# Optimization experiments

Hardware: AMD Instinct MI355X
Metric: run time of the kernel (lower is better)

## Reference

```python
import jax, jax.numpy as jnp
import numpy as np
import math

N = 50000
E = 600000
HID = 128
NG = 50
NF = 128
CUTOFF = 10.0
OFFSET = 0.0


def ssp(x):
    # shifted softplus, standard SchNet activation
    return jax.nn.softplus(x) - jnp.log(2.0).astype(x.dtype)


def setup_inputs() -> dict:
    key = jax.random.key(0)
    ks = jax.random.split(key, 12)
    x = jax.random.normal(ks[0], (N, HID), dtype=jnp.float32)
    ji_pairs = jax.random.randint(ks[1], (2, E), 0, N, dtype=jnp.int64)
    e_ji = jax.random.uniform(ks[2], (E,), dtype=jnp.float32) * CUTOFF
    e_ji_basis = jax.random.normal(ks[3], (E, NG), dtype=jnp.float32)
    # filter_nn: Linear(NG, NF) -> ssp -> Linear(NF, NF)
    fw1 = jax.random.normal(ks[4], (NF, NG), dtype=jnp.float32) * (1.0 / np.sqrt(NG))
    fb1 = jnp.zeros((NF,), jnp.float32)
    fw2 = jax.random.normal(ks[5], (NF, NF), dtype=jnp.float32) * (1.0 / np.sqrt(NF))
    fb2 = jnp.zeros((NF,), jnp.float32)
    # CFConv linear1 (no bias), linear2
    w1 = jax.random.normal(ks[6], (NF, HID), dtype=jnp.float32) * (1.0 / np.sqrt(HID))
    w2 = jax.random.normal(ks[7], (HID, NF), dtype=jnp.float32) * (1.0 / np.sqrt(NF))
    b2 = jnp.zeros((HID,), jnp.float32)
    # InteractionBlock linear3
    w3 = jax.random.normal(ks[8], (HID, HID), dtype=jnp.float32) * (1.0 / np.sqrt(HID))
    b3 = jnp.zeros((HID,), jnp.float32)
    return {"x": x, "ji_pairs": ji_pairs, "e_ji": e_ji, "e_ji_basis": e_ji_basis,
            "fw1": fw1, "fb1": fb1, "fw2": fw2, "fb2": fb2,
            "w1": w1, "w2": w2, "b2": b2, "w3": w3, "b3": b3}


def reference(x, ji_pairs, e_ji, e_ji_basis, fw1, fb1, fw2, fb2, w1, w2, b2, w3, b3):
    # cosine cutoff  [E]
    C = 0.25 * (jnp.cos((e_ji - OFFSET) * (np.pi / (CUTOFF - OFFSET))) + 1.0)
    # filter MLP on edge basis  [E, NF]
    h = ssp(e_ji_basis @ fw1.T + fb1)
    W = (h @ fw2.T + fb2) * C[:, None]
    # node projection  [N, NF]
    xh = x @ w1.T
    # gather x_j, modulate by W, scatter-add to target nodes (PyG source_to_target)
    src, dst = ji_pairs[0], ji_pairs[1]
    msg = xh[src] * W                                # [E, NF]
    agg = jax.ops.segment_sum(msg, dst, num_segments=N)  # [N, NF]
    out = agg @ w2.T + b2                            # [N, HID]
    out = ssp(out)
    out = out @ w3.T + b3
    return out
```

## Files before the change

### kernel.cpp

```cpp
#include <hip/hip_runtime.h>

typedef float f32x4 __attribute__((ext_vector_type(4)));
typedef short bf16x8 __attribute__((ext_vector_type(8)));
typedef unsigned short u16;
typedef unsigned int u32;

__device__ __forceinline__ u32 cvt_pk_bf16(float lo, float hi) {
    u32 r;
    asm("v_cvt_pk_bf16_f32 %0, %1, %2" : "=v"(r) : "v"(lo), "v"(hi));
    return r;
}

__device__ __forceinline__ u16 f2b(float f) {
    union { float f; u32 u; } v; v.f = f;
    u32 r = v.u + 0x7fffu + ((v.u >> 16) & 1u);
    return (u16)(r >> 16);
}
__device__ __forceinline__ float b2f_lo(u32 p) {
    union { u32 u; float f; } v; v.u = p << 16; return v.f;
}
__device__ __forceinline__ float b2f_hi(u32 p) {
    union { u32 u; float f; } v; v.u = p & 0xffff0000u; return v.f;
}

__device__ __forceinline__ float ssp(float x) {
    return fmaxf(x, 0.0f) + __logf(1.0f + __expf(-fabsf(x))) - 0.6931471805599453f;
}

__global__ void prep_weights(const float* __restrict__ fw1,
                             const float* __restrict__ fw2,
                             const float* __restrict__ w1,
                             const float* __restrict__ w2,
                             const float* __restrict__ w3,
                             u16* __restrict__ out) {
    int t = blockIdx.x * blockDim.x + threadIdx.x;
    if (t < 128 * 64) {
        int c = t >> 6, k = t & 63;
        out[t] = f2b(k < 50 ? fw1[c * 50 + k] : 0.0f);
        return;
    }
    t -= 128 * 64;
    if (t < 16384) { out[8192 + t] = f2b(fw2[t]); return; }
    t -= 16384;
    if (t < 16384) { out[8192 + 16384 + t] = f2b(w1[t]); return; }
    t -= 16384;
    if (t < 16384) { out[8192 + 32768 + t] = f2b(w2[t]); return; }
    t -= 16384;
    if (t < 16384) { out[8192 + 49152 + t] = f2b(w3[t]); return; }
}

template <int ACT, int OBF>
__global__ __launch_bounds__(256, 3) void linear128(
    const float* __restrict__ in, const u16* __restrict__ wb,
    const float* __restrict__ bias, void* __restrict__ outv, int M) {
    __shared__ u16 in_lds[64 * 136];
    __shared__ u16 w_lds[128 * 136];

    const int tid = threadIdx.x;
    const int r0 = blockIdx.x * 64;

    for (int idx = tid; idx < 128 * 16; idx += 256) {
        int c = idx >> 4, kc = (idx & 15) * 8;
        *reinterpret_cast<uint4*>(&w_lds[c * 136 + kc]) =
            *reinterpret_cast<const uint4*>(&wb[c * 128 + kc]);
    }
    for (int idx = tid; idx < 64 * 32; idx += 256) {
        int r = idx >> 5, kc = (idx & 31) * 4;
        int row = r0 + r;
        float4 v = make_float4(0.f, 0.f, 0.f, 0.f);
        if (row < M) v = *reinterpret_cast<const float4*>(&in[(size_t)row * 128 + kc]);
        u32* p = reinterpret_cast<u32*>(&in_lds[r * 136 + kc]);
        p[0] = cvt_pk_bf16(v.x, v.y); p[1] = cvt_pk_bf16(v.z, v.w);
    }
    __syncthreads();

    const int l = tid & 63, w = tid >> 6;
    const int lr = l & 15, lg = l >> 4;

    f32x4 acc[8] = {};
    for (int ks = 0; ks < 4; ++ks) {
        bf16x8 a = *reinterpret_cast<const bf16x8*>(
            &in_lds[(w * 16 + lr) * 136 + ks * 32 + lg * 8]);
        for (int n = 0; n < 8; ++n) {
            bf16x8 b = *reinterpret_cast<const bf16x8*>(
                &w_lds[(n * 16 + lr) * 136 + ks * 32 + lg * 8]);
            acc[n] = __builtin_amdgcn_mfma_f32_16x16x32_bf16(a, b, acc[n], 0, 0, 0);
        }
    }

    for (int n = 0; n < 8; ++n) {
        int c = n * 16 + lr;
        float bv = bias ? bias[c] : 0.0f;
        for (int i = 0; i < 4; ++i) {
            int row = r0 + w * 16 + lg * 4 + i;
            if (row < M) {
                float v = acc[n][i] + bv;
                if (ACT) v = ssp(v);
                if (OBF) ((u16*)outv)[(size_t)row * 128 + c] = f2b(v);
                else     ((float*)outv)[(size_t)row * 128 + c] = v;
            }
        }
    }
}

__global__ __launch_bounds__(512) void edge_mlp(
    const float* __restrict__ basis, const float* __restrict__ e_ji,
    const u16* __restrict__ fw1b, const u16* __restrict__ fw2b,
    const float* __restrict__ fb1, const float* __restrict__ fb2,
    const int* __restrict__ epos, u16* __restrict__ Wb,
    int E, int nTiles, int stride) {
    __shared__ u16 bas[2][32 * 72];
    __shared__ u16 hb[2][32 * 136];

    const int tid = threadIdx.x;
    const int l = tid & 63, w = tid >> 6;
    const int lr = l & 15, lg = l >> 4;
    const int c8 = lg * 8, c4 = lg * 4;

    bf16x8 wa1[2], wa2[4];
    const u16* p1 = &fw1b[(size_t)(w * 16 + lr) * 64];
    wa1[0] = *reinterpret_cast<const bf16x8*>(p1 + c8);
    wa1[1] = *reinterpret_cast<const bf16x8*>(p1 + 32 + c8);
    const u16* p2 = &fw2b[(size_t)(w * 16 + lr) * 128];
#pragma unroll
    for (int ks = 0; ks < 4; ++ks)
        wa2[ks] = *reinterpret_cast<const bf16x8*>(p2 + ks * 32 + c8);
    const float4 b1v = *reinterpret_cast<const float4*>(&fb1[w * 16 + c4]);
    const float4 b2v = *reinterpret_cast<const float4*>(&fb2[w * 16 + c4]);

    for (int idx = tid; idx < 2 * 32 * 7; idx += 512) {
        int b = idx / 224, rem = idx - b * 224;
        int row = rem / 7, q = rem - row * 7;
        *reinterpret_cast<u32*>(&bas[b][row * 72 + 50 + 2 * q]) = 0u;
    }

    const int srow = tid & 31, cb = tid >> 5;
    const bool has2 = cb < 9;

    int it = blockIdx.x;
    if (it >= nTiles) return;

    {
        int er = it * 32 + srow; if (er >= E) er = E - 1;
        const float* rp = &basis[(size_t)er * 50];
        float2 v0 = *reinterpret_cast<const float2*>(rp + 2 * cb);
        *reinterpret_cast<u32*>(&bas[0][srow * 72 + 2 * cb]) = cvt_pk_bf16(v0.x, v0.y);
        if (has2) {
            float2 v1 = *reinterpret_cast<const float2*>(rp + 2 * (cb + 16));
            *reinterpret_cast<u32*>(&bas[0][srow * 72 + 2 * (cb + 16)]) =
                cvt_pk_bf16(v1.x, v1.y);
        }
    }
    __syncthreads();

    int buf = 0;
    for (; it < nTiles; it += stride, buf ^= 1) {
        const int nxt = it + stride;
        const bool hn = nxt < nTiles;
        float2 stg0, stg1;
        if (hn) {
            int er = nxt * 32 + srow; if (er >= E) er = E - 1;
            const float* rp = &basis[(size_t)er * 50];
            stg0 = *reinterpret_cast<const float2*>(rp + 2 * cb);
            if (has2) stg1 = *reinterpret_cast<const float2*>(rp + 2 * (cb + 16));
        }
        const int er0 = it * 32 + lr, er1 = er0 + 16;
        const int ec0 = er0 < E ? er0 : E - 1;
        const int ec1 = er1 < E ? er1 : E - 1;
        const int ep0 = epos[ec0], ep1 = epos[ec1];
        const float ej0 = e_ji[ec0], ej1 = e_ji[ec1];

        f32x4 acc1[2] = {};
#pragma unroll
        for (int ks = 0; ks < 2; ++ks) {
            bf16x8 bb0 = *reinterpret_cast<const bf16x8*>(
                &bas[buf][lr * 72 + ks * 32 + c8]);
            bf16x8 bb1 = *reinterpret_cast<const bf16x8*>(
                &bas[buf][(16 + lr) * 72 + ks * 32 + c8]);
            acc1[0] = __builtin_amdgcn_mfma_f32_16x16x32_bf16(wa1[ks], bb0, acc1[0], 0, 0, 0);
            acc1[1] = __builtin_amdgcn_mfma_f32_16x16x32_bf16(wa1[ks], bb1, acc1[1], 0, 0, 0);
        }
#pragma unroll
        for (int t = 0; t < 2; ++t) {
            u32* d = reinterpret_cast<u32*>(
                &hb[buf][(t * 16 + lr) * 136 + w * 16 + c4]);
            d[0] = cvt_pk_bf16(ssp(acc1[t][0] + b1v.x), ssp(acc1[t][1] + b1v.y));
            d[1] = cvt_pk_bf16(ssp(acc1[t][2] + b1v.z), ssp(acc1[t][3] + b1v.w));
        }
        if (hn) {
            *reinterpret_cast<u32*>(&bas[buf ^ 1][srow * 72 + 2 * cb]) =
                cvt_pk_bf16(stg0.x, stg0.y);
            if (has2)
                *reinterpret_cast<u32*>(&bas[buf ^ 1][srow * 72 + 2 * (cb + 16)]) =
                    cvt_pk_bf16(stg1.x, stg1.y);
        }
        __syncthreads();

        f32x4 acc2[2] = {};
#pragma unroll
        for (int ks = 0; ks < 4; ++ks) {
            bf16x8 hb0 = *reinterpret_cast<const bf16x8*>(
                &hb[buf][lr * 136 + ks * 32 + c8]);
            bf16x8 hb1 = *reinterpret_cast<const bf16x8*>(
                &hb[buf][(16 + lr) * 136 + ks * 32 + c8]);
            acc2[0] = __builtin_amdgcn_mfma_f32_16x16x32_bf16(wa2[ks], hb0, acc2[0], 0, 0, 0);
            acc2[1] = __builtin_amdgcn_mfma_f32_16x16x32_bf16(wa2[ks], hb1, acc2[1], 0, 0, 0);
        }
#pragma unroll
        for (int t = 0; t < 2; ++t) {
            const int er = t == 0 ? er0 : er1;
            if (er < E) {
                const float ej = t == 0 ? ej0 : ej1;
                const int pos = t == 0 ? ep0 : ep1;
                const float cv = 0.25f * (__cosf(ej * 0.31415926535897932f) + 1.0f);
                uint2 pk;
                pk.x = cvt_pk_bf16((acc2[t][0] + b2v.x) * cv,
                                   (acc2[t][1] + b2v.y) * cv);
                pk.y = cvt_pk_bf16((acc2[t][2] + b2v.z) * cv,
                                   (acc2[t][3] + b2v.w) * cv);
                *reinterpret_cast<uint2*>(
                    &Wb[(size_t)pos * 128 + w * 16 + c4]) = pk;
            }
        }
    }
}

__global__ __launch_bounds__(256) void fused_tail(
    const u16* __restrict__ aggb, const u16* __restrict__ w2b,
    const u16* __restrict__ w3b, const float* __restrict__ b2,
    const float* __restrict__ b3, float* __restrict__ out,
    int N, int nTiles, int stride) {
    __shared__ u16 bas[2][32 * 136];
    __shared__ u16 hb[2][32 * 136];

    const int tid = threadIdx.x;
    const int l = tid & 63, w = tid >> 6;
    const int lr = l & 15, lg = l >> 4;
    const int c8 = lg * 8, c4 = lg * 4;

    bf16x8 wA[2][4], wB[2][4];
    float4 b2v[2], b3v[2];
#pragma unroll
    for (int i = 0; i < 2; ++i) {
        const u16* pA = &w2b[(size_t)((w * 2 + i) * 16 + lr) * 128];
        const u16* pB = &w3b[(size_t)((w * 2 + i) * 16 + lr) * 128];
#pragma unroll
        for (int ks = 0; ks < 4; ++ks) {
            wA[i][ks] = *reinterpret_cast<const bf16x8*>(pA + ks * 32 + c8);
            wB[i][ks] = *reinterpret_cast<const bf16x8*>(pB + ks * 32 + c8);
        }
        b2v[i] = *reinterpret_cast<const float4*>(&b2[(w * 2 + i) * 16 + c4]);
        b3v[i] = *reinterpret_cast<const float4*>(&b3[(w * 2 + i) * 16 + c4]);
    }

    const int srow = tid & 31, cb = tid >> 5;

    int it = blockIdx.x;
    if (it >= nTiles) return;

    {
        int nd = it * 32 + srow; if (nd >= N) nd = N - 1;
        *reinterpret_cast<uint4*>(&bas[0][srow * 136 + cb * 8]) =
            *reinterpret_cast<const uint4*>(&aggb[(size_t)nd * 128 + cb * 8]);
        *reinterpret_cast<uint4*>(&bas[0][srow * 136 + 64 + cb * 8]) =
            *reinterpret_cast<const uint4*>(&aggb[(size_t)nd * 128 + 64 + cb * 8]);
    }
    __syncthreads();

    int buf = 0;
    for (; it < nTiles; it += stride, buf ^= 1) {
        const int nxt = it + stride;
        const bool hn = nxt < nTiles;
        uint4 stg0, stg1;
        if (hn) {
            int nd = nxt * 32 + srow; if (nd >= N) nd = N - 1;
            stg0 = *reinterpret_cast<const uint4*>(&aggb[(size_t)nd * 128 + cb * 8]);
            stg1 = *reinterpret_cast<const uint4*>(&aggb[(size_t)nd * 128 + 64 + cb * 8]);
        }

        f32x4 acc1[2][2] = {};
#pragma unroll
        for (int ks = 0; ks < 4; ++ks) {
            bf16x8 bb0 = *reinterpret_cast<const bf16x8*>(
                &bas[buf][lr * 136 + ks * 32 + c8]);
            bf16x8 bb1 = *reinterpret_cast<const bf16x8*>(
                &bas[buf][(16 + lr) * 136 + ks * 32 + c8]);
#pragma unroll
            for (int i = 0; i < 2; ++i) {
                acc1[0][i] = __builtin_amdgcn_mfma_f32_16x16x32_bf16(wA[i][ks], bb0, acc1[0][i], 0, 0, 0);
                acc1[1][i] = __builtin_amdgcn_mfma_f32_16x16x32_bf16(wA[i][ks], bb1, acc1[1][i], 0, 0, 0);
            }
        }
#pragma unroll
        for (int t = 0; t < 2; ++t) {
#pragma unroll
            for (int i = 0; i < 2; ++i) {
                u32* d = reinterpret_cast<u32*>(
                    &hb[buf][(t * 16 + lr) * 136 + (w * 2 + i) * 16 + c4]);
                d[0] = cvt_pk_bf16(ssp(acc1[t][i][0] + b2v[i].x),
                                   ssp(acc1[t][i][1] + b2v[i].y));
                d[1] = cvt_pk_bf16(ssp(acc1[t][i][2] + b2v[i].z),
                                   ssp(acc1[t][i][3] + b2v[i].w));
            }
        }
        if (hn) {
            *reinterpret_cast<uint4*>(&bas[buf ^ 1][srow * 136 + cb * 8]) = stg0;
            *reinterpret_cast<uint4*>(&bas[buf ^ 1][srow * 136 + 64 + cb * 8]) = stg1;
        }
        __syncthreads();

        f32x4 acc2[2][2] = {};
#pragma unroll
        for (int ks = 0; ks < 4; ++ks) {
            bf16x8 hb0 = *reinterpret_cast<const bf16x8*>(
                &hb[buf][lr * 136 + ks * 32 + c8]);
            bf16x8 hb1 = *reinterpret_cast<const bf16x8*>(
                &hb[buf][(16 + lr) * 136 + ks * 32 + c8]);
#pragma unroll
            for (int i = 0; i < 2; ++i) {
                acc2[0][i] = __builtin_amdgcn_mfma_f32_16x16x32_bf16(wB[i][ks], hb0, acc2[0][i], 0, 0, 0);
                acc2[1][i] = __builtin_amdgcn_mfma_f32_16x16x32_bf16(wB[i][ks], hb1, acc2[1][i], 0, 0, 0);
            }
        }
#pragma unroll
        for (int t = 0; t < 2; ++t) {
            int nd = it * 32 + t * 16 + lr;
            if (nd < N) {
#pragma unroll
                for (int i = 0; i < 2; ++i) {
                    float4 o;
                    o.x = acc2[t][i][0] + b3v[i].x;
                    o.y = acc2[t][i][1] + b3v[i].y;
                    o.z = acc2[t][i][2] + b3v[i].z;
                    o.w = acc2[t][i][3] + b3v[i].w;
                    *reinterpret_cast<float4*>(
                        &out[(size_t)nd * 128 + (w * 2 + i) * 16 + c4]) = o;
                }
            }
        }
    }
}

__global__ void hist_kernel(const int* __restrict__ pairs, int* __restrict__ deg, int E) {
    int e = blockIdx.x * blockDim.x + threadIdx.x;
    if (e < E) atomicAdd(&deg[pairs[E + e]], 1);
}

__global__ void scan_a(const int* __restrict__ deg, int* __restrict__ incl,
                       int* __restrict__ bsum, int N) {
    __shared__ int s[256];
    int i = blockIdx.x * 256 + threadIdx.x;
    int v = (i < N) ? deg[i] : 0;
    s[threadIdx.x] = v; __syncthreads();
    for (int off = 1; off < 256; off <<= 1) {
        int t = (threadIdx.x >= off) ? s[threadIdx.x - off] : 0;
        __syncthreads();
        s[threadIdx.x] += t; __syncthreads();
    }
    if (i < N) incl[i] = s[threadIdx.x];
    if (threadIdx.x == 255) bsum[blockIdx.x] = s[255];
}

__global__ void scan_b(int* __restrict__ bsum, int nb) {
    __shared__ int s[256];
    int v = (threadIdx.x < nb) ? bsum[threadIdx.x] : 0;
    s[threadIdx.x] = v; __syncthreads();
    for (int off = 1; off < 256; off <<= 1) {
        int t = (threadIdx.x >= off) ? s[threadIdx.x - off] : 0;
        __syncthreads();
        s[threadIdx.x] += t; __syncthreads();
    }
    if (threadIdx.x < nb) bsum[threadIdx.x] = s[threadIdx.x] - v;
}

__global__ void scan_c(const int* __restrict__ incl, const int* __restrict__ deg,
                       const int* __restrict__ bsum, int* __restrict__ rowst,
                       int* __restrict__ cursor, int N) {
    int i = blockIdx.x * 256 + threadIdx.x;
    if (i < N) {
        int r = incl[i] - deg[i] + bsum[blockIdx.x];
        rowst[i] = r; cursor[i] = r;
    }
}

__global__ void fill_kernel(const int* __restrict__ pairs, int* __restrict__ cursor,
                            int* __restrict__ esrc, int* __restrict__ epos, int E) {
    int e = blockIdx.x * blockDim.x + threadIdx.x;
    if (e < E) {
        int s = pairs[e], d = pairs[E + e];
        int pos = atomicAdd(&cursor[d], 1);
        esrc[pos] = s;
        epos[e] = pos;
    }
}

__global__ __launch_bounds__(256) void aggregate(
    const u16* __restrict__ Wb, const u16* __restrict__ xhb,
    const int* __restrict__ rowst, const int* __restrict__ deg,
    const int* __restrict__ esrc, u16* __restrict__ aggb, int N) {
    const int w = threadIdx.x >> 6, lane = threadIdx.x & 63;
    const int n = blockIdx.x * 4 + w;
    if (n >= N) return;
    const int rs = rowst[n], d = deg[n];
    const int g = lane >> 4;
    const int co = (lane & 15) * 8;
    float acc[8] = {0.f, 0.f, 0.f, 0.f, 0.f, 0.f, 0.f, 0.f};
    const int nq = (d + 3) >> 2;
    const int dm1 = d > 0 ? d - 1 : 0;

    int srcn = (d > 0) ? esrc[rs + (g < d ? g : dm1)] : 0;
    for (int q = 0; q < nq; ++q) {
        const int k = q * 4 + g;
        const bool val = k < d;
        const int row = rs + (val ? k : dm1);
        const int src = srcn;
        const int kn = (q + 1) * 4 + g;
        if (q + 1 < nq) srcn = esrc[rs + (kn < d ? kn : dm1)];

        uint4 wp = *reinterpret_cast<const uint4*>(&Wb[(size_t)row * 128 + co]);
        uint4 xp = *reinterpret_cast<const uint4*>(&xhb[(size_t)src * 128 + co]);
        if (val) {
            const u32* wu = reinterpret_cast<const u32*>(&wp);
            const u32* xu = reinterpret_cast<const u32*>(&xp);
#pragma unroll
            for (int c = 0; c < 4; ++c) {
                acc[2 * c]     = fmaf(b2f_lo(xu[c]), b2f_lo(wu[c]), acc[2 * c]);
                acc[2 * c + 1] = fmaf(b2f_hi(xu[c]), b2f_hi(wu[c]), acc[2 * c + 1]);
            }
        }
    }
#pragma unroll
    for (int c = 0; c < 8; ++c) {
        float v = acc[c];
        v += __shfl_xor(v, 16);
        v += __shfl_xor(v, 32);
        acc[c] = v;
    }
    if (g == 0) {
        uint4 pk;
        pk.x = cvt_pk_bf16(acc[0], acc[1]);
        pk.y = cvt_pk_bf16(acc[2], acc[3]);
        pk.z = cvt_pk_bf16(acc[4], acc[5]);
        pk.w = cvt_pk_bf16(acc[6], acc[7]);
        *reinterpret_cast<uint4*>(&aggb[(size_t)n * 128 + co]) = pk;
    }
}

__global__ __launch_bounds__(256, 2) void edge_kernel(
    const float* __restrict__ basis, const float* __restrict__ e_ji,
    const int* __restrict__ pairs, const float* __restrict__ xh,
    const u16* __restrict__ fw1b, const u16* __restrict__ fw2b,
    const float* __restrict__ fb1, const float* __restrict__ fb2,
    float* __restrict__ agg, int E) {
    __shared__ u16 hb[64 * 136];
    __shared__ u16 fw1_lds[128 * 72];
    __shared__ u16 fw2_lds[128 * 136];
    __shared__ float cc[64];
    __shared__ int s_src[64];
    __shared__ int s_dst[64];

    const int tid = threadIdx.x;
    const int e0 = blockIdx.x * 64;

    for (int idx = tid; idx < 128 * 8; idx += 256) {
        int c = idx >> 3, kc = (idx & 7) * 8;
        *reinterpret_cast<uint4*>(&fw1_lds[c * 72 + kc]) =
            *reinterpret_cast<const uint4*>(&fw1b[c * 64 + kc]);
    }
    for (int idx = tid; idx < 128 * 16; idx += 256) {
        int c = idx >> 4, kc = (idx & 15) * 8;
        *reinterpret_cast<uint4*>(&fw2_lds[c * 136 + kc]) =
            *reinterpret_cast<const uint4*>(&fw2b[c * 128 + kc]);
    }
    for (int idx = tid; idx < 64 * 64; idx += 256) {
        int e = idx >> 6, k = idx & 63;
        int eg = e0 + e;
        float v = (k < 50 && eg < E) ? basis[(size_t)eg * 50 + k] : 0.0f;
        hb[e * 72 + k] = f2b(v);
    }
    if (tid < 64) {
        int eg = e0 + tid;
        if (eg < E) {
            cc[tid] = 0.25f * (__cosf(e_ji[eg] * 0.31415926535897932f) + 1.0f);
            s_src[tid] = pairs[eg];
            s_dst[tid] = pairs[E + eg];
        } else { cc[tid] = 0.0f; s_src[tid] = 0; s_dst[tid] = 0; }
    }
    __syncthreads();

    const int l = tid & 63, w = tid >> 6;
    const int lr = l & 15, lg = l >> 4;

    f32x4 acc1[8] = {};
    for (int ks = 0; ks < 2; ++ks) {
        bf16x8 a = *reinterpret_cast<const bf16x8*>(
            &hb[(w * 16 + lr) * 72 + ks * 32 + lg * 8]);
        for (int n = 0; n < 8; ++n) {
            bf16x8 b = *reinterpret_cast<const bf16x8*>(
                &fw1_lds[(n * 16 + lr) * 72 + ks * 32 + lg * 8]);
            acc1[n] = __builtin_amdgcn_mfma_f32_16x16x32_bf16(a, b, acc1[n], 0, 0, 0);
        }
    }
    __syncthreads();

    for (int n = 0; n < 8; ++n) {
        int c = n * 16 + lr;
        float bv = fb1[c];
        for (int i = 0; i < 4; ++i) {
            int r = w * 16 + lg * 4 + i;
            hb[r * 136 + c] = f2b(ssp(acc1[n][i] + bv));
        }
    }
    __syncthreads();

    f32x4 acc2[8] = {};
    for (int ks = 0; ks < 4; ++ks) {
        bf16x8 a = *reinterpret_cast<const bf16x8*>(
            &hb[(w * 16 + lr) * 136 + ks * 32 + lg * 8]);
        for (int n = 0; n < 8; ++n) {
            bf16x8 b = *reinterpret_cast<const bf16x8*>(
                &fw2_lds[(n * 16 + lr) * 136 + ks * 32 + lg * 8]);
            acc2[n] = __builtin_amdgcn_mfma_f32_16x16x32_bf16(a, b, acc2[n], 0, 0, 0);
        }
    }

    for (int n = 0; n < 8; ++n) {
        int c = n * 16 + lr;
        float bv = fb2[c];
        for (int i = 0; i < 4; ++i) {
            int eloc = w * 16 + lg * 4 + i;
            if (e0 + eloc < E) {
                float Wv = (acc2[n][i] + bv) * cc[eloc];
                float val = xh[(size_t)s_src[eloc] * 128 + c] * Wv;
                unsafeAtomicAdd(&agg[(size_t)s_dst[eloc] * 128 + c], val);
            }
        }
    }
}

extern "C" void kernel_launch(void* const* d_in, const int* in_sizes, int n_in,
                              void* d_out, int out_size, void* d_ws, size_t ws_size,
                              hipStream_t stream) {
    const float* x      = (const float*)d_in[0];
    const int*   pairs  = (const int*)d_in[1];
    const float* e_ji   = (const float*)d_in[2];
    const float* basis  = (const float*)d_in[3];
    const float* fw1    = (const float*)d_in[4];
    const float* fb1    = (const float*)d_in[5];
    const float* fw2    = (const float*)d_in[6];
    const float* fb2    = (const float*)d_in[7];
    const float* w1     = (const float*)d_in[8];
    const float* w2     = (const float*)d_in[9];
    const float* b2     = (const float*)d_in[10];
    const float* w3     = (const float*)d_in[11];
    const float* b3     = (const float*)d_in[12];
    float* out = (float*)d_out;

    const int N = in_sizes[0] / 128;
    const int E = in_sizes[2];
    const int nodeBlocks = (N + 63) / 64;
    const int nchunks = (N + 255) / 256;
    char* ws = (char*)d_ws;

    size_t off = 0;
    auto nxt = [&](size_t bytes) {
        size_t o = off; off = (off + bytes + 255) & ~(size_t)255; return o;
    };
    u16*   Wb     = (u16*)  (ws + nxt((size_t)E * 128 * 2));
    u16*   xhb    = (u16*)  (ws + nxt((size_t)N * 128 * 2));
    u16*   aggb   = (u16*)  (ws + nxt((size_t)N * 128 * 2));
    u16*   wb     = (u16*)  (ws + nxt(81920 * 2));
    int*   deg    = (int*)  (ws + nxt((size_t)N * 4));
    int*   incl   = (int*)  (ws + nxt((size_t)N * 4));
    int*   rowst  = (int*)  (ws + nxt((size_t)N * 4));
    int*   cursor = (int*)  (ws + nxt((size_t)N * 4));
    int*   bsum   = (int*)  (ws + nxt(1024));
    int*   esrc   = (int*)  (ws + nxt((size_t)E * 4));
    int*   epos   = (int*)  (ws + nxt((size_t)E * 4));
    const size_t needed = off;

    const u16* fw1b = wb;
    const u16* fw2b = wb + 8192;
    const u16* w1b  = wb + 8192 + 16384;
    const u16* w2b  = wb + 8192 + 32768;
    const u16* w3b  = wb + 8192 + 49152;

    if (ws_size >= needed && nchunks <= 256) {
        prep_weights<<<288, 256, 0, stream>>>(fw1, fw2, w1, w2, w3, wb);
        hipMemsetAsync(deg, 0, (size_t)N * 4, stream);

        linear128<0, 1><<<nodeBlocks, 256, 0, stream>>>(x, w1b, nullptr, xhb, N);

        hist_kernel<<<(E + 255) / 256, 256, 0, stream>>>(pairs, deg, E);
        scan_a<<<nchunks, 256, 0, stream>>>(deg, incl, bsum, N);
        scan_b<<<1, 256, 0, stream>>>(bsum, nchunks);
        scan_c<<<nchunks, 256, 0, stream>>>(incl, deg, bsum, rowst, cursor, N);
        fill_kernel<<<(E + 255) / 256, 256, 0, stream>>>(pairs, cursor, esrc, epos, E);

        const int nTiles = (E + 31) / 32;
        const int gridE = nTiles < 1024 ? nTiles : 1024;
        edge_mlp<<<gridE, 512, 0, stream>>>(basis, e_ji, fw1b, fw2b,
                                            fb1, fb2, epos, Wb, E, nTiles, gridE);

        aggregate<<<(N + 3) / 4, 256, 0, stream>>>(Wb, xhb, rowst, deg,
                                                   esrc, aggb, N);

        const int ntT = (N + 31) / 32;
        const int gridT = ntT < 1024 ? ntT : 1024;
        fused_tail<<<gridT, 256, 0, stream>>>(aggb, w2b, w3b, b2, b3, out,
                                              N, ntT, gridT);
    } else {
        const size_t nodeBytes = (size_t)N * 128 * sizeof(float);
        float* xhf   = (float*)ws;
        float* aggf  = (float*)(ws + nodeBytes);
        u16*   wbf   = (u16*)(ws + 2 * nodeBytes);
        const u16* ffw1b = wbf;
        const u16* ffw2b = wbf + 8192;
        const u16* fw1bw = wbf + 8192 + 16384;
        const u16* fw2bw = wbf + 8192 + 32768;
        const u16* fw3bw = wbf + 8192 + 49152;

        prep_weights<<<288, 256, 0, stream>>>(fw1, fw2, w1, w2, w3, wbf);
        hipMemsetAsync(aggf, 0, nodeBytes, stream);
        linear128<0, 0><<<nodeBlocks, 256, 0, stream>>>(x, fw1bw, nullptr, xhf, N);
        edge_kernel<<<(E + 63) / 64, 256, 0, stream>>>(basis, e_ji, pairs, xhf,
                                                       ffw1b, ffw2b, fb1, fb2, aggf, E);
        linear128<1, 0><<<nodeBlocks, 256, 0, stream>>>(aggf, fw2bw, b2, out, N);
        linear128<0, 0><<<nodeBlocks, 256, 0, stream>>>(out, fw3bw, b3, out, N);
    }
}
```

Baseline: 264.6 us.

## Fuse source-node gather and message multiply into edge MLP epilogue

The edge MLP now gathers the projected source-node features itself and writes the full message (xh[src] * W) in CSR order. The aggregate kernel then only sums message rows, so it no longer needs the esrc index array or a second random gather, and the fill kernel stops writing esrc. The cost is that edge_mlp does random gathers of xh (small uint2 reads per lane) in its hot loop, and the product is rounded to bf16 once before summation.

```diff
diff --git a/kernel.cpp b/kernel.cpp
--- a/kernel.cpp
+++ b/kernel.cpp
@@ -105,9 +105,10 @@
 
 __global__ __launch_bounds__(512) void edge_mlp(
     const float* __restrict__ basis, const float* __restrict__ e_ji,
+    const int* __restrict__ pairs, const u16* __restrict__ xhb,
     const u16* __restrict__ fw1b, const u16* __restrict__ fw2b,
     const float* __restrict__ fb1, const float* __restrict__ fb2,
-    const int* __restrict__ epos, u16* __restrict__ Wb,
+    const int* __restrict__ epos, u16* __restrict__ Mb,
     int E, int nTiles, int stride) {
     __shared__ u16 bas[2][32 * 72];
     __shared__ u16 hb[2][32 * 136];
@@ -169,6 +170,11 @@
         const int ec1 = er1 < E ? er1 : E - 1;
         const int ep0 = epos[ec0], ep1 = epos[ec1];
         const float ej0 = e_ji[ec0], ej1 = e_ji[ec1];
+        const int src0 = pairs[ec0], src1 = pairs[ec1];
+        const uint2 xv0 = *reinterpret_cast<const uint2*>(
+            &xhb[(size_t)src0 * 128 + w * 16 + c4]);
+        const uint2 xv1 = *reinterpret_cast<const uint2*>(
+            &xhb[(size_t)src1 * 128 + w * 16 + c4]);
 
         f32x4 acc1[2] = {};
 #pragma unroll
@@ -212,14 +218,17 @@
             if (er < E) {
                 const float ej = t == 0 ? ej0 : ej1;
                 const int pos = t == 0 ? ep0 : ep1;
+                const uint2 xv = t == 0 ? xv0 : xv1;
                 const float cv = 0.25f * (__cosf(ej * 0.31415926535897932f) + 1.0f);
+                float m0 = b2f_lo(xv.x) * ((acc2[t][0] + b2v.x) * cv);
+                float m1 = b2f_hi(xv.x) * ((acc2[t][1] + b2v.y) * cv);
+                float m2 = b2f_lo(xv.y) * ((acc2[t][2] + b2v.z) * cv);
+                float m3 = b2f_hi(xv.y) * ((acc2[t][3] + b2v.w) * cv);
                 uint2 pk;
-                pk.x = cvt_pk_bf16((acc2[t][0] + b2v.x) * cv,
-                                   (acc2[t][1] + b2v.y) * cv);
-                pk.y = cvt_pk_bf16((acc2[t][2] + b2v.z) * cv,
-                                   (acc2[t][3] + b2v.w) * cv);
+                pk.x = cvt_pk_bf16(m0, m1);
+                pk.y = cvt_pk_bf16(m2, m3);
                 *reinterpret_cast<uint2*>(
-                    &Wb[(size_t)pos * 128 + w * 16 + c4]) = pk;
+                    &Mb[(size_t)pos * 128 + w * 16 + c4]) = pk;
             }
         }
     }
@@ -384,20 +393,18 @@
 }
 
 __global__ void fill_kernel(const int* __restrict__ pairs, int* __restrict__ cursor,
-                            int* __restrict__ esrc, int* __restrict__ epos, int E) {
+                            int* __restrict__ epos, int E) {
     int e = blockIdx.x * blockDim.x + threadIdx.x;
     if (e < E) {
-        int s = pairs[e], d = pairs[E + e];
+        int d = pairs[E + e];
         int pos = atomicAdd(&cursor[d], 1);
-        esrc[pos] = s;
         epos[e] = pos;
     }
 }
 
 __global__ __launch_bounds__(256) void aggregate(
-    const u16* __restrict__ Wb, const u16* __restrict__ xhb,
-    const int* __restrict__ rowst, const int* __restrict__ deg,
-    const int* __restrict__ esrc, u16* __restrict__ aggb, int N) {
+    const u16* __restrict__ Mb, const int* __restrict__ rowst,
+    const int* __restrict__ deg, u16* __restrict__ aggb, int N) {
     const int w = threadIdx.x >> 6, lane = threadIdx.x & 63;
     const int n = blockIdx.x * 4 + w;
     if (n >= N) return;
@@ -408,24 +415,17 @@
     const int nq = (d + 3) >> 2;
     const int dm1 = d > 0 ? d - 1 : 0;
 
-    int srcn = (d > 0) ? esrc[rs + (g < d ? g : dm1)] : 0;
     for (int q = 0; q < nq; ++q) {
         const int k = q * 4 + g;
         const bool val = k < d;
         const int row = rs + (val ? k : dm1);
-        const int src = srcn;
-        const int kn = (q + 1) * 4 + g;
-        if (q + 1 < nq) srcn = esrc[rs + (kn < d ? kn : dm1)];
-
-        uint4 wp = *reinterpret_cast<const uint4*>(&Wb[(size_t)row * 128 + co]);
-        uint4 xp = *reinterpret_cast<const uint4*>(&xhb[(size_t)src * 128 + co]);
+        uint4 mp = *reinterpret_cast<const uint4*>(&Mb[(size_t)row * 128 + co]);
         if (val) {
-            const u32* wu = reinterpret_cast<const u32*>(&wp);
-            const u32* xu = reinterpret_cast<const u32*>(&xp);
+            const u32* mu = reinterpret_cast<const u32*>(&mp);
 #pragma unroll
             for (int c = 0; c < 4; ++c) {
-                acc[2 * c]     = fmaf(b2f_lo(xu[c]), b2f_lo(wu[c]), acc[2 * c]);
-                acc[2 * c + 1] = fmaf(b2f_hi(xu[c]), b2f_hi(wu[c]), acc[2 * c + 1]);
+                acc[2 * c]     += b2f_lo(mu[c]);
+                acc[2 * c + 1] += b2f_hi(mu[c]);
             }
         }
     }
@@ -566,7 +566,7 @@
     auto nxt = [&](size_t bytes) {
         size_t o = off; off = (off + bytes + 255) & ~(size_t)255; return o;
     };
-    u16*   Wb     = (u16*)  (ws + nxt((size_t)E * 128 * 2));
+    u16*   Mb     = (u16*)  (ws + nxt((size_t)E * 128 * 2));
     u16*   xhb    = (u16*)  (ws + nxt((size_t)N * 128 * 2));
     u16*   aggb   = (u16*)  (ws + nxt((size_t)N * 128 * 2));
     u16*   wb     = (u16*)  (ws + nxt(81920 * 2));
@@ -575,7 +575,6 @@
     int*   rowst  = (int*)  (ws + nxt((size_t)N * 4));
     int*   cursor = (int*)  (ws + nxt((size_t)N * 4));
     int*   bsum   = (int*)  (ws + nxt(1024));
-    int*   esrc   = (int*)  (ws + nxt((size_t)E * 4));
     int*   epos   = (int*)  (ws + nxt((size_t)E * 4));
     const size_t needed = off;
 
@@ -595,15 +594,14 @@
         scan_a<<<nchunks, 256, 0, stream>>>(deg, incl, bsum, N);
         scan_b<<<1, 256, 0, stream>>>(bsum, nchunks);
         scan_c<<<nchunks, 256, 0, stream>>>(incl, deg, bsum, rowst, cursor, N);
-        fill_kernel<<<(E + 255) / 256, 256, 0, stream>>>(pairs, cursor, esrc, epos, E);
+        fill_kernel<<<(E + 255) / 256, 256, 0, stream>>>(pairs, cursor, epos, E);
 
         const int nTiles = (E + 31) / 32;
         const int gridE = nTiles < 1024 ? nTiles : 1024;
-        edge_mlp<<<gridE, 512, 0, stream>>>(basis, e_ji, fw1b, fw2b,
-                                            fb1, fb2, epos, Wb, E, nTiles, gridE);
-
-        aggregate<<<(N + 3) / 4, 256, 0, stream>>>(Wb, xhb, rowst, deg,
-                                                   esrc, aggb, N);
+        edge_mlp<<<gridE, 512, 0, stream>>>(basis, e_ji, pairs, xhb, fw1b, fw2b,
+                                            fb1, fb2, epos, Mb, E, nTiles, gridE);
+
+        aggregate<<<(N + 3) / 4, 256, 0, stream>>>(Mb, rowst, deg, aggb, N);
 
         const int ntT = (N + 31) / 32;
         const int gridT = ntT < 1024 ? ntT : 1024;
```

After: 271.2 us. 1.03x slower.
